# Optimization experiments

Measured on AMD Instinct MI355X. Metric: run time of the kernel, lower is better.

## Reference

```python
import jax, jax.numpy as jnp
import numpy as np

N_NODES = 100000
N_EDGES = 500000
H = 128

def _mlp(x, w1, b1, w2, b2):
    return jax.nn.relu(x @ w1 + b1) @ w2 + b2

def setup_inputs() -> dict:
    key = jax.random.key(0)
    ks = jax.random.split(key, 20)
    s = lambda fan_in: 1.0 / np.sqrt(fan_in)
    inp = {
        'x': jax.random.normal(ks[0], (N_NODES, H), jnp.float32),
        'edge_index': jax.random.randint(ks[1], (2, N_EDGES), 0, N_NODES, jnp.int64),
        'edge_attr': jax.random.normal(ks[2], (N_EDGES, H), jnp.float32),
        # edge_mlp: Linear(3h->h), ReLU, Linear(h->h); weights stored [in,out]
        'ew1': jax.random.uniform(ks[3], (3 * H, H), jnp.float32, -s(3 * H), s(3 * H)),
        'eb1': jnp.zeros((H,), jnp.float32),
        'ew2': jax.random.uniform(ks[4], (H, H), jnp.float32, -s(H), s(H)),
        'eb2': jnp.zeros((H,), jnp.float32),
        # node_mlp_phi: Linear(2h->h), ReLU, Linear(h->h)
        'pw1': jax.random.uniform(ks[5], (2 * H, H), jnp.float32, -s(2 * H), s(2 * H)),
        'pb1': jnp.zeros((H,), jnp.float32),
        'pw2': jax.random.uniform(ks[6], (H, H), jnp.float32, -s(H), s(H)),
        'pb2': jnp.zeros((H,), jnp.float32),
        # node_mlp_gamma: Linear(2h->h), ReLU, Linear(h->h)
        'gw1': jax.random.uniform(ks[7], (2 * H, H), jnp.float32, -s(2 * H), s(2 * H)),
        'gb1': jnp.zeros((H,), jnp.float32),
        'gw2': jax.random.uniform(ks[8], (H, H), jnp.float32, -s(H), s(H)),
        'gb2': jnp.zeros((H,), jnp.float32),
        # node_mlp_beta: Linear(h->h), ReLU, Linear(h->h)
        'bw1': jax.random.uniform(ks[9], (H, H), jnp.float32, -s(H), s(H)),
        'bb1': jnp.zeros((H,), jnp.float32),
        'bw2': jax.random.uniform(ks[10], (H, H), jnp.float32, -s(H), s(H)),
        'bb2': jnp.zeros((H,), jnp.float32),
    }
    return inp

def reference(x, edge_index, edge_attr, ew1, eb1, ew2, eb2, pw1, pb1, pw2, pb2,
              gw1, gb1, gw2, gb2, bw1, bb1, bw2, bb2):
    n = x.shape[0]
    row, col = edge_index[0], edge_index[1]
    x_row = x[row]            # [E, h]
    x_col = x[col]            # [E, h]
    edge_feat = jnp.concatenate([x_row, x_col, edge_attr], axis=1)  # [E, 3h]
    new_edge_attr = _mlp(edge_feat, ew1, eb1, ew2, eb2)             # [E, h]
    messages = _mlp(jnp.concatenate([x_col, new_edge_attr], axis=1), pw1, pb1, pw2, pb2)  # [E, h]
    # scatter_mean over row -> [N, h]
    sums = jax.ops.segment_sum(messages, row, num_segments=n)
    counts = jax.ops.segment_sum(jnp.ones((messages.shape[0],), messages.dtype), row, num_segments=n)
    agg = sums / jnp.maximum(counts, 1.0)[:, None]
    node_feat = jnp.concatenate([x, agg], axis=1)                   # [N, 2h]
    x_new = _mlp(node_feat, gw1, gb1, gw2, gb2)
    x_new = x_new + _mlp(x_new, bw1, bb1, bw2, bb2)
    return (x_new, new_edge_attr)
```

## Files before the change

### kernel.cpp

```cpp
#include <hip/hip_runtime.h>
#include <hip/hip_bf16.h>

typedef float f32x4 __attribute__((ext_vector_type(4)));
typedef short bf16x8 __attribute__((ext_vector_type(8)));
typedef unsigned short u16;
typedef unsigned short u16x4 __attribute__((ext_vector_type(4)));

#define HDIM 128
#define NNODES 100000
#define NEDGES 500000

#define WT_OFF   0
#define P1_OFF   393216
#define P2_OFF   (P1_OFF + 25600000)
#define Q_OFF    (P2_OFF + 25600000)
#define SUMS_OFF (Q_OFF + 25600000)
#define CNT_OFF  (SUMS_OFF + 51200000)

__device__ __forceinline__ u16 f2bf(float f) {
  unsigned int u = __builtin_bit_cast(unsigned int, f);
  u += 0x7fffu + ((u >> 16) & 1u);
  return (u16)(u >> 16);
}
__device__ __forceinline__ float bf2f(u16 h) {
  unsigned int u = ((unsigned int)h) << 16;
  return __builtin_bit_cast(float, u);
}

__device__ __forceinline__ u16* lds_at(u16* base, int row, int colBytes) {
  return (u16*)((char*)base + row * 256 + (colBytes ^ ((row & 7) << 4)));
}

__device__ __forceinline__ void stage_weight(const u16* __restrict__ wsrc, u16* wb, int tid) {
#pragma unroll
  for (int i = 0; i < 8; ++i) {
    int q = tid + 256 * i;
    int r = q >> 4, c = q & 15;
    uint4 v = *(const uint4*)(wsrc + r * 128 + c * 8);
    *(uint4*)lds_at(wb, r, c * 16) = v;
  }
}

__device__ __forceinline__ void wave_gemm(u16* aBuf, u16* wb, f32x4* acc, int lane, int wv) {
  const int arow = 16 * wv + (lane & 15);
  const int kg = (lane >> 4) * 16;
#pragma unroll
  for (int ks = 0; ks < 4; ++ks) {
    bf16x8 a = *(const bf16x8*)lds_at(aBuf, arow, ks * 64 + kg);
#pragma unroll
    for (int nt = 0; nt < 8; ++nt) {
      bf16x8 b = *(const bf16x8*)lds_at(wb, nt * 16 + (lane & 15), ks * 64 + kg);
      acc[nt] = __builtin_amdgcn_mfma_f32_16x16x32_bf16(a, b, acc[nt], 0, 0, 0);
    }
  }
}

__global__ __launch_bounds__(256) void k_prep(
    const float* __restrict__ ew1, const float* __restrict__ ew2,
    const float* __restrict__ pw1, const float* __restrict__ pw2,
    const float* __restrict__ gw1, const float* __restrict__ gw2,
    const float* __restrict__ bw1, const float* __restrict__ bw2,
    u16* __restrict__ WT) {
  int m = blockIdx.x;
  const float* src; int k0 = 0;
  switch (m) {
    case 0: src = ew1; k0 = 0;   break;
    case 1: src = ew1; k0 = 128; break;
    case 2: src = ew1; k0 = 256; break;
    case 3: src = ew2; break;
    case 4: src = pw1; break;
    case 5: src = pw1; k0 = 128; break;
    case 6: src = pw2; break;
    case 7: src = gw1; break;
    case 8: src = gw1; k0 = 128; break;
    case 9: src = gw2; break;
    case 10: src = bw1; break;
    default: src = bw2; break;
  }
  for (int i = 0; i < 64; ++i) {
    int idx = threadIdx.x + 256 * i;
    int n = idx & 127, k = idx >> 7;
    WT[m * 16384 + n * 128 + k] = f2bf(src[(k0 + k) * 128 + n]);
  }
}

__global__ __launch_bounds__(256) void k_node_pre(
    const float* __restrict__ x, const u16* __restrict__ WT,
    const float* __restrict__ eb1, const float* __restrict__ pb1,
    u16* __restrict__ P1, u16* __restrict__ P2, u16* __restrict__ Qm) {
  __shared__ u16 smem[32768];
  u16* wb = smem; u16* bufX = smem + 16384; u16* bufO = smem + 24576;
  const int tid = threadIdx.x, lane = tid & 63, wv = tid >> 6;
  const int nbase = blockIdx.x * 64 + 16 * wv;
#pragma unroll
  for (int i = 0; i < 8; ++i) {
    int q = lane + 64 * i; int r = q >> 5, c4 = q & 31; int n = nbase + r;
    float4 v = make_float4(0.f, 0.f, 0.f, 0.f);
    if (n < NNODES) v = *(const float4*)(x + (size_t)n * HDIM + c4 * 4);
    u16x4 h = { f2bf(v.x), f2bf(v.y), f2bf(v.z), f2bf(v.w) };
    *(u16x4*)lds_at(bufX, 16 * wv + r, c4 * 8) = h;
  }
#pragma unroll 1
  for (int job = 0; job < 3; ++job) {
    int m = (job == 0) ? 0 : (job == 1) ? 1 : 4;
    const float* bias = (job == 0) ? eb1 : (job == 1) ? nullptr : pb1;
    u16* out = (job == 0) ? P1 : (job == 1) ? P2 : Qm;
    __syncthreads();
    stage_weight(WT + m * 16384, wb, tid);
    __syncthreads();
    f32x4 acc[8] = {};
    wave_gemm(bufX, wb, acc, lane, wv);
#pragma unroll
    for (int nt = 0; nt < 8; ++nt) {
      int col = nt * 16 + (lane & 15);
      float bv = bias ? bias[col] : 0.0f;
#pragma unroll
      for (int j = 0; j < 4; ++j) {
        int r = 4 * (lane >> 4) + j;
        *lds_at(bufO, 16 * wv + r, col * 2) = f2bf(acc[nt][j] + bv);
      }
    }
#pragma unroll
    for (int i = 0; i < 4; ++i) {
      int q = lane + 64 * i; int r = q >> 4, c = q & 15; int n = nbase + r;
      if (n < NNODES)
        *(bf16x8*)(out + (size_t)n * HDIM + c * 8) =
            *(const bf16x8*)lds_at(bufO, 16 * wv + r, c * 16);
    }
  }
}

__global__ __launch_bounds__(256) void k_edge(
    const float* __restrict__ attr, const int* __restrict__ eidx,
    const u16* __restrict__ WT, const u16* __restrict__ P1,
    const u16* __restrict__ P2, const u16* __restrict__ Qm,
    const float* __restrict__ eb2, float* __restrict__ sums,
    float* __restrict__ counts, float* __restrict__ outNE) {
  __shared__ u16 smem[32768];
  u16* wb = smem; u16* bufA = smem + 16384; u16* bufH = smem + 24576;
  const int tid = threadIdx.x, lane = tid & 63, wv = tid >> 6;
  const int e0 = blockIdx.x * 64;
  const int ebase = e0 + 16 * wv;
  if (tid < 64 && e0 + tid < NEDGES) atomicAdd(&counts[eidx[e0 + tid]], 1.0f);
#pragma unroll
  for (int i = 0; i < 8; ++i) {
    int q = lane + 64 * i; int r = q >> 5, c4 = q & 31; int e = ebase + r;
    float4 v = make_float4(0.f, 0.f, 0.f, 0.f);
    if (e < NEDGES) v = *(const float4*)(attr + (size_t)e * HDIM + c4 * 4);
    u16x4 h = { f2bf(v.x), f2bf(v.y), f2bf(v.z), f2bf(v.w) };
    *(u16x4*)lds_at(bufA, 16 * wv + r, c4 * 8) = h;
  }
  stage_weight(WT + 2 * 16384, wb, tid);
  __syncthreads();
  f32x4 acc[8] = {};
  wave_gemm(bufA, wb, acc, lane, wv);
#pragma unroll
  for (int i = 0; i < 4; ++i) {
    int q = lane + 64 * i; int r = q >> 4, cc = (q & 15) * 8; int e = ebase + r;
    bf16x8 res = {};
    if (e < NEDGES) {
      int rid = eidx[e], cid = eidx[NEDGES + e];
      bf16x8 a = *(const bf16x8*)(P1 + (size_t)rid * HDIM + cc);
      bf16x8 b = *(const bf16x8*)(P2 + (size_t)cid * HDIM + cc);
#pragma unroll
      for (int k = 0; k < 8; ++k)
        res[k] = (short)f2bf(bf2f((u16)a[k]) + bf2f((u16)b[k]));
    }
    *(bf16x8*)lds_at(bufH, 16 * wv + r, cc * 2) = res;
  }
#pragma unroll
  for (int nt = 0; nt < 8; ++nt) {
#pragma unroll
    for (int j = 0; j < 4; ++j) {
      int r = 4 * (lane >> 4) + j; int cb = (nt * 16 + (lane & 15)) * 2;
      u16* p = lds_at(bufH, 16 * wv + r, cb);
      float v = acc[nt][j] + bf2f(*p);
      *p = f2bf(fmaxf(v, 0.0f));
    }
  }
  __syncthreads();
  stage_weight(WT + 3 * 16384, wb, tid);
  __syncthreads();
#pragma unroll
  for (int t = 0; t < 8; ++t) acc[t] = (f32x4){0.f, 0.f, 0.f, 0.f};
  wave_gemm(bufH, wb, acc, lane, wv);
#pragma unroll
  for (int nt = 0; nt < 8; ++nt) {
    int col = nt * 16 + (lane & 15);
    float bias = eb2[col];
#pragma unroll
    for (int j = 0; j < 4; ++j) {
      int r = 4 * (lane >> 4) + j; int e = ebase + r;
      float v = acc[nt][j] + bias;
      *lds_at(bufA, 16 * wv + r, col * 2) = f2bf(v);
      if (e < NEDGES) outNE[(size_t)e * HDIM + col] = v;
    }
  }
#pragma unroll
  for (int i = 0; i < 4; ++i) {
    int q = lane + 64 * i; int r = q >> 4, cc = (q & 15) * 8; int e = ebase + r;
    bf16x8 res = {};
    if (e < NEDGES) res = *(const bf16x8*)(Qm + (size_t)eidx[NEDGES + e] * HDIM + cc);
    *(bf16x8*)lds_at(bufH, 16 * wv + r, cc * 2) = res;
  }
  __syncthreads();
  stage_weight(WT + 5 * 16384, wb, tid);
  __syncthreads();
#pragma unroll
  for (int t = 0; t < 8; ++t) acc[t] = (f32x4){0.f, 0.f, 0.f, 0.f};
  wave_gemm(bufA, wb, acc, lane, wv);
  int rid4[4];
#pragma unroll
  for (int j = 0; j < 4; ++j) {
    int e = ebase + 4 * (lane >> 4) + j;
    rid4[j] = (e < NEDGES) ? eidx[e] : -1;
  }
#pragma unroll
  for (int nt = 0; nt < 8; ++nt) {
    int col = nt * 16 + (lane & 15);
#pragma unroll
    for (int j = 0; j < 4; ++j) {
      if (rid4[j] >= 0) {
        int r = 4 * (lane >> 4) + j;
        float v = acc[nt][j] + bf2f(*lds_at(bufH, 16 * wv + r, col * 2));
        v = fmaxf(v, 0.0f);
        atomicAdd(&sums[(size_t)rid4[j] * HDIM + col], v);
      }
    }
  }
}

__global__ __launch_bounds__(256) void k_node(
    const float* __restrict__ x, const u16* __restrict__ WT,
    const float* __restrict__ sums, const float* __restrict__ counts,
    const float* __restrict__ pb2, const float* __restrict__ gb1,
    const float* __restrict__ gb2, const float* __restrict__ bb1,
    const float* __restrict__ bb2, float* __restrict__ dout) {
  __shared__ u16 smem[32768];
  u16* wb = smem; u16* bufA = smem + 16384; u16* bufH = smem + 24576;
  const int tid = threadIdx.x, lane = tid & 63, wv = tid >> 6;
  const int nbase = blockIdx.x * 64 + 16 * wv;
#pragma unroll
  for (int i = 0; i < 8; ++i) {
    int q = lane + 64 * i; int r = q >> 5, c4 = q & 31; int n = nbase + r;
    float4 v = make_float4(0.f, 0.f, 0.f, 0.f);
    if (n < NNODES) v = *(const float4*)(sums + (size_t)n * HDIM + c4 * 4);
    u16x4 h = { f2bf(v.x), f2bf(v.y), f2bf(v.z), f2bf(v.w) };
    *(u16x4*)lds_at(bufA, 16 * wv + r, c4 * 8) = h;
  }
  stage_weight(WT + 6 * 16384, wb, tid);
  __syncthreads();
  f32x4 acc[8] = {};
  wave_gemm(bufA, wb, acc, lane, wv);
  float cv[4];
#pragma unroll
  for (int j = 0; j < 4; ++j) {
    int n = nbase + 4 * (lane >> 4) + j;
    cv[j] = (n < NNODES) ? counts[n] : 0.0f;
  }
#pragma unroll
  for (int nt = 0; nt < 8; ++nt) {
    int col = nt * 16 + (lane & 15);
    float bias = pb2[col];
#pragma unroll
    for (int j = 0; j < 4; ++j) {
      int r = 4 * (lane >> 4) + j;
      float v = (cv[j] >= 1.0f) ? (acc[nt][j] / cv[j] + bias) : 0.0f;
      *lds_at(bufH, 16 * wv + r, col * 2) = f2bf(v);
    }
  }
#pragma unroll
  for (int i = 0; i < 8; ++i) {
    int q = lane + 64 * i; int r = q >> 5, c4 = q & 31; int n = nbase + r;
    float4 v = make_float4(0.f, 0.f, 0.f, 0.f);
    if (n < NNODES) v = *(const float4*)(x + (size_t)n * HDIM + c4 * 4);
    u16x4 h = { f2bf(v.x), f2bf(v.y), f2bf(v.z), f2bf(v.w) };
    *(u16x4*)lds_at(bufA, 16 * wv + r, c4 * 8) = h;
  }
  __syncthreads();
  stage_weight(WT + 7 * 16384, wb, tid);
  __syncthreads();
  f32x4 acc2[8] = {};
  wave_gemm(bufA, wb, acc2, lane, wv);
  __syncthreads();
  stage_weight(WT + 8 * 16384, wb, tid);
  __syncthreads();
  wave_gemm(bufH, wb, acc2, lane, wv);
#pragma unroll
  for (int nt = 0; nt < 8; ++nt) {
    int col = nt * 16 + (lane & 15);
    float bias = gb1[col];
#pragma unroll
    for (int j = 0; j < 4; ++j) {
      int r = 4 * (lane >> 4) + j;
      *lds_at(bufH, 16 * wv + r, col * 2) = f2bf(fmaxf(acc2[nt][j] + bias, 0.0f));
    }
  }
  __syncthreads();
  stage_weight(WT + 9 * 16384, wb, tid);
  __syncthreads();
  f32x4 accX[8] = {};
  wave_gemm(bufH, wb, accX, lane, wv);
#pragma unroll
  for (int nt = 0; nt < 8; ++nt) {
    int col = nt * 16 + (lane & 15);
    float bias = gb2[col];
#pragma unroll
    for (int j = 0; j < 4; ++j) {
      int r = 4 * (lane >> 4) + j;
      accX[nt][j] += bias;
      *lds_at(bufA, 16 * wv + r, col * 2) = f2bf(accX[nt][j]);
    }
  }
  __syncthreads();
  stage_weight(WT + 10 * 16384, wb, tid);
  __syncthreads();
  f32x4 acc3[8] = {};
  wave_gemm(bufA, wb, acc3, lane, wv);
#pragma unroll
  for (int nt = 0; nt < 8; ++nt) {
    int col = nt * 16 + (lane & 15);
    float bias = bb1[col];
#pragma unroll
    for (int j = 0; j < 4; ++j) {
      int r = 4 * (lane >> 4) + j;
      *lds_at(bufH, 16 * wv + r, col * 2) = f2bf(fmaxf(acc3[nt][j] + bias, 0.0f));
    }
  }
  __syncthreads();
  stage_weight(WT + 11 * 16384, wb, tid);
  __syncthreads();
  f32x4 acc4[8] = {};
  wave_gemm(bufH, wb, acc4, lane, wv);
#pragma unroll
  for (int nt = 0; nt < 8; ++nt) {
    int col = nt * 16 + (lane & 15);
    float bias = bb2[col];
#pragma unroll
    for (int j = 0; j < 4; ++j) {
      int n = nbase + 4 * (lane >> 4) + j;
      if (n < NNODES) dout[(size_t)n * HDIM + col] = accX[nt][j] + acc4[nt][j] + bias;
    }
  }
}

extern "C" void kernel_launch(void* const* d_in, const int* in_sizes, int n_in,
                              void* d_out, int out_size, void* d_ws, size_t ws_size,
                              hipStream_t stream) {
  (void)in_sizes; (void)n_in; (void)out_size; (void)ws_size;
  const float* x   = (const float*)d_in[0];
  const int* eidx  = (const int*)d_in[1];
  const float* attr= (const float*)d_in[2];
  const float* ew1 = (const float*)d_in[3];
  const float* eb1 = (const float*)d_in[4];
  const float* ew2 = (const float*)d_in[5];
  const float* eb2 = (const float*)d_in[6];
  const float* pw1 = (const float*)d_in[7];
  const float* pb1 = (const float*)d_in[8];
  const float* pw2 = (const float*)d_in[9];
  const float* pb2 = (const float*)d_in[10];
  const float* gw1 = (const float*)d_in[11];
  const float* gb1 = (const float*)d_in[12];
  const float* gw2 = (const float*)d_in[13];
  const float* gb2 = (const float*)d_in[14];
  const float* bw1 = (const float*)d_in[15];
  const float* bb1 = (const float*)d_in[16];
  const float* bw2 = (const float*)d_in[17];
  const float* bb2 = (const float*)d_in[18];

  char* ws = (char*)d_ws;
  u16* WT   = (u16*)(ws + WT_OFF);
  u16* P1   = (u16*)(ws + P1_OFF);
  u16* P2   = (u16*)(ws + P2_OFF);
  u16* Qm   = (u16*)(ws + Q_OFF);
  float* sums   = (float*)(ws + SUMS_OFF);
  float* counts = (float*)(ws + CNT_OFF);
  float* xnew_out = (float*)d_out;
  float* ne_out   = (float*)d_out + (size_t)NNODES * HDIM;

  hipMemsetAsync(ws + SUMS_OFF, 0, 51200000 + 400000, stream);
  k_prep<<<12, 256, 0, stream>>>(ew1, ew2, pw1, pw2, gw1, gw2, bw1, bw2, WT);
  k_node_pre<<<1563, 256, 0, stream>>>(x, WT, eb1, pb1, P1, P2, Qm);
  k_edge<<<7813, 256, 0, stream>>>(attr, eidx, WT, P1, P2, Qm, eb2, sums, counts, ne_out);
  k_node<<<1563, 256, 0, stream>>>(x, WT, sums, counts, pb2, gb1, gb2, bb1, bb2, xnew_out);
}
```

Before: 1.066 ms.

## Read weights from global in MFMA loop, use packed fp16 atomics for sums

The GEMM helper now loads weight fragments straight from global memory (served by L1/L2) instead of staging each 128x128 weight into LDS. This removes the staging loops and many __syncthreads, and halves LDS use per block, which may allow more resident blocks. The scatter-sum accumulator becomes fp16 with global_atomic_pk_add_f16, halving atomic count and the memset size, at the cost of fp16 accumulation precision and range. The weight-prep kernel is also parallelized over 96 blocks with vectorized stores.

```diff
diff --git a/kernel.cpp b/kernel.cpp
--- a/kernel.cpp
+++ b/kernel.cpp
@@ -1,5 +1,6 @@
 #include <hip/hip_runtime.h>
 #include <hip/hip_bf16.h>
+#include <hip/hip_fp16.h>
 
 typedef float f32x4 __attribute__((ext_vector_type(4)));
 typedef short bf16x8 __attribute__((ext_vector_type(8)));
@@ -15,7 +16,7 @@
 #define P2_OFF   (P1_OFF + 25600000)
 #define Q_OFF    (P2_OFF + 25600000)
 #define SUMS_OFF (Q_OFF + 25600000)
-#define CNT_OFF  (SUMS_OFF + 51200000)
+#define CNT_OFF  (SUMS_OFF + 25600000)
 
 __device__ __forceinline__ u16 f2bf(float f) {
   unsigned int u = __builtin_bit_cast(unsigned int, f);
@@ -31,25 +32,20 @@
   return (u16*)((char*)base + row * 256 + (colBytes ^ ((row & 7) << 4)));
 }
 
-__device__ __forceinline__ void stage_weight(const u16* __restrict__ wsrc, u16* wb, int tid) {
-#pragma unroll
-  for (int i = 0; i < 8; ++i) {
-    int q = tid + 256 * i;
-    int r = q >> 4, c = q & 15;
-    uint4 v = *(const uint4*)(wsrc + r * 128 + c * 8);
-    *(uint4*)lds_at(wb, r, c * 16) = v;
-  }
-}
-
-__device__ __forceinline__ void wave_gemm(u16* aBuf, u16* wb, f32x4* acc, int lane, int wv) {
-  const int arow = 16 * wv + (lane & 15);
-  const int kg = (lane >> 4) * 16;
+__device__ __forceinline__ void atomic_pk_add_f16(__half* addr, unsigned int data) {
+  asm volatile("global_atomic_pk_add_f16 %0, %1, off" :: "v"(addr), "v"(data) : "memory");
+}
+
+__device__ __forceinline__ void wave_gemm_g(u16* aBuf, const u16* __restrict__ wt,
+                                            f32x4* acc, int lane, int wv) {
+  const int m = lane & 15, kq = lane >> 4;
+  const int arow = 16 * wv + m;
 #pragma unroll
   for (int ks = 0; ks < 4; ++ks) {
-    bf16x8 a = *(const bf16x8*)lds_at(aBuf, arow, ks * 64 + kg);
+    bf16x8 a = *(const bf16x8*)lds_at(aBuf, arow, ks * 64 + kq * 16);
 #pragma unroll
     for (int nt = 0; nt < 8; ++nt) {
-      bf16x8 b = *(const bf16x8*)lds_at(wb, nt * 16 + (lane & 15), ks * 64 + kg);
+      bf16x8 b = *(const bf16x8*)(wt + (size_t)(nt * 16 + m) * 128 + ks * 32 + kq * 8);
       acc[nt] = __builtin_amdgcn_mfma_f32_16x16x32_bf16(a, b, acc[nt], 0, 0, 0);
     }
   }
@@ -61,7 +57,7 @@
     const float* __restrict__ gw1, const float* __restrict__ gw2,
     const float* __restrict__ bw1, const float* __restrict__ bw2,
     u16* __restrict__ WT) {
-  int m = blockIdx.x;
+  int m = blockIdx.x >> 3;
   const float* src; int k0 = 0;
   switch (m) {
     case 0: src = ew1; k0 = 0;   break;
@@ -77,19 +73,21 @@
     case 10: src = bw1; break;
     default: src = bw2; break;
   }
-  for (int i = 0; i < 64; ++i) {
-    int idx = threadIdx.x + 256 * i;
-    int n = idx & 127, k = idx >> 7;
-    WT[m * 16384 + n * 128 + k] = f2bf(src[(k0 + k) * 128 + n]);
-  }
+  int c = (blockIdx.x & 7) * 256 + threadIdx.x;
+  int n = c >> 4, kc = c & 15;
+  u16 w8[8];
+#pragma unroll
+  for (int t = 0; t < 8; ++t)
+    w8[t] = f2bf(src[(size_t)(k0 + kc * 8 + t) * 128 + n]);
+  *(uint4*)(WT + m * 16384 + n * 128 + kc * 8) = *(const uint4*)w8;
 }
 
 __global__ __launch_bounds__(256) void k_node_pre(
     const float* __restrict__ x, const u16* __restrict__ WT,
     const float* __restrict__ eb1, const float* __restrict__ pb1,
     u16* __restrict__ P1, u16* __restrict__ P2, u16* __restrict__ Qm) {
-  __shared__ u16 smem[32768];
-  u16* wb = smem; u16* bufX = smem + 16384; u16* bufO = smem + 24576;
+  __shared__ u16 smem[16384];
+  u16* bufX = smem; u16* bufO = smem + 8192;
   const int tid = threadIdx.x, lane = tid & 63, wv = tid >> 6;
   const int nbase = blockIdx.x * 64 + 16 * wv;
 #pragma unroll
@@ -102,14 +100,11 @@
   }
 #pragma unroll 1
   for (int job = 0; job < 3; ++job) {
-    int m = (job == 0) ? 0 : (job == 1) ? 1 : 4;
+    int mw = (job == 0) ? 0 : (job == 1) ? 1 : 4;
     const float* bias = (job == 0) ? eb1 : (job == 1) ? nullptr : pb1;
     u16* out = (job == 0) ? P1 : (job == 1) ? P2 : Qm;
-    __syncthreads();
-    stage_weight(WT + m * 16384, wb, tid);
-    __syncthreads();
     f32x4 acc[8] = {};
-    wave_gemm(bufX, wb, acc, lane, wv);
+    wave_gemm_g(bufX, WT + mw * 16384, acc, lane, wv);
 #pragma unroll
     for (int nt = 0; nt < 8; ++nt) {
       int col = nt * 16 + (lane & 15);
@@ -134,10 +129,10 @@
     const float* __restrict__ attr, const int* __restrict__ eidx,
     const u16* __restrict__ WT, const u16* __restrict__ P1,
     const u16* __restrict__ P2, const u16* __restrict__ Qm,
-    const float* __restrict__ eb2, float* __restrict__ sums,
+    const float* __restrict__ eb2, __half* __restrict__ sums,
     float* __restrict__ counts, float* __restrict__ outNE) {
-  __shared__ u16 smem[32768];
-  u16* wb = smem; u16* bufA = smem + 16384; u16* bufH = smem + 24576;
+  __shared__ u16 smem[16384];
+  u16* bufA = smem; u16* bufH = smem + 8192;
   const int tid = threadIdx.x, lane = tid & 63, wv = tid >> 6;
   const int e0 = blockIdx.x * 64;
   const int ebase = e0 + 16 * wv;
@@ -150,10 +145,8 @@
     u16x4 h = { f2bf(v.x), f2bf(v.y), f2bf(v.z), f2bf(v.w) };
     *(u16x4*)lds_at(bufA, 16 * wv + r, c4 * 8) = h;
   }
-  stage_weight(WT + 2 * 16384, wb, tid);
-  __syncthreads();
   f32x4 acc[8] = {};
-  wave_gemm(bufA, wb, acc, lane, wv);
+  wave_gemm_g(bufA, WT + 2 * 16384, acc, lane, wv);
 #pragma unroll
   for (int i = 0; i < 4; ++i) {
     int q = lane + 64 * i; int r = q >> 4, cc = (q & 15) * 8; int e = ebase + r;
@@ -178,12 +171,9 @@
       *p = f2bf(fmaxf(v, 0.0f));
     }
   }
-  __syncthreads();
-  stage_weight(WT + 3 * 16384, wb, tid);
-  __syncthreads();
 #pragma unroll
   for (int t = 0; t < 8; ++t) acc[t] = (f32x4){0.f, 0.f, 0.f, 0.f};
-  wave_gemm(bufH, wb, acc, lane, wv);
+  wave_gemm_g(bufH, WT + 3 * 16384, acc, lane, wv);
 #pragma unroll
   for (int nt = 0; nt < 8; ++nt) {
     int col = nt * 16 + (lane & 15);
@@ -203,12 +193,9 @@
     if (e < NEDGES) res = *(const bf16x8*)(Qm + (size_t)eidx[NEDGES + e] * HDIM + cc);
     *(bf16x8*)lds_at(bufH, 16 * wv + r, cc * 2) = res;
   }
-  __syncthreads();
-  stage_weight(WT + 5 * 16384, wb, tid);
-  __syncthreads();
 #pragma unroll
   for (int t = 0; t < 8; ++t) acc[t] = (f32x4){0.f, 0.f, 0.f, 0.f};
-  wave_gemm(bufA, wb, acc, lane, wv);
+  wave_gemm_g(bufA, WT + 5 * 16384, acc, lane, wv);
   int rid4[4];
 #pragma unroll
   for (int j = 0; j < 4; ++j) {
@@ -220,11 +207,16 @@
     int col = nt * 16 + (lane & 15);
 #pragma unroll
     for (int j = 0; j < 4; ++j) {
-      if (rid4[j] >= 0) {
-        int r = 4 * (lane >> 4) + j;
-        float v = acc[nt][j] + bf2f(*lds_at(bufH, 16 * wv + r, col * 2));
-        v = fmaxf(v, 0.0f);
-        atomicAdd(&sums[(size_t)rid4[j] * HDIM + col], v);
+      int r = 4 * (lane >> 4) + j;
+      float v = acc[nt][j] + bf2f(*lds_at(bufH, 16 * wv + r, col * 2));
+      v = fmaxf(v, 0.0f);
+      float other = __shfl_xor(v, 1);
+      if (((lane & 1) == (j & 1)) && rid4[j] >= 0) {
+        float lo = ((lane & 1) == 0) ? v : other;
+        float hi = ((lane & 1) == 0) ? other : v;
+        __half2 h2 = __floats2half2_rn(lo, hi);
+        atomic_pk_add_f16(sums + (size_t)rid4[j] * HDIM + (col & ~1),
+                          __builtin_bit_cast(unsigned int, h2));
       }
     }
   }
@@ -232,26 +224,31 @@
 
 __global__ __launch_bounds__(256) void k_node(
     const float* __restrict__ x, const u16* __restrict__ WT,
-    const float* __restrict__ sums, const float* __restrict__ counts,
+    const __half* __restrict__ sums, const float* __restrict__ counts,
     const float* __restrict__ pb2, const float* __restrict__ gb1,
     const float* __restrict__ gb2, const float* __restrict__ bb1,
     const float* __restrict__ bb2, float* __restrict__ dout) {
-  __shared__ u16 smem[32768];
-  u16* wb = smem; u16* bufA = smem + 16384; u16* bufH = smem + 24576;
+  __shared__ u16 smem[16384];
+  u16* bufA = smem; u16* bufH = smem + 8192;
   const int tid = threadIdx.x, lane = tid & 63, wv = tid >> 6;
   const int nbase = blockIdx.x * 64 + 16 * wv;
 #pragma unroll
-  for (int i = 0; i < 8; ++i) {
-    int q = lane + 64 * i; int r = q >> 5, c4 = q & 31; int n = nbase + r;
-    float4 v = make_float4(0.f, 0.f, 0.f, 0.f);
-    if (n < NNODES) v = *(const float4*)(sums + (size_t)n * HDIM + c4 * 4);
-    u16x4 h = { f2bf(v.x), f2bf(v.y), f2bf(v.z), f2bf(v.w) };
-    *(u16x4*)lds_at(bufA, 16 * wv + r, c4 * 8) = h;
-  }
-  stage_weight(WT + 6 * 16384, wb, tid);
-  __syncthreads();
+  for (int i = 0; i < 4; ++i) {
+    int q = lane + 64 * i; int r = q >> 4, c8 = q & 15; int n = nbase + r;
+    bf16x8 h = {};
+    if (n < NNODES) {
+      const __half2* sp = (const __half2*)(sums + (size_t)n * HDIM + c8 * 8);
+#pragma unroll
+      for (int t = 0; t < 4; ++t) {
+        float2 f = __half22float2(sp[t]);
+        h[2 * t]     = (short)f2bf(f.x);
+        h[2 * t + 1] = (short)f2bf(f.y);
+      }
+    }
+    *(bf16x8*)lds_at(bufA, 16 * wv + r, c8 * 16) = h;
+  }
   f32x4 acc[8] = {};
-  wave_gemm(bufA, wb, acc, lane, wv);
+  wave_gemm_g(bufA, WT + 6 * 16384, acc, lane, wv);
   float cv[4];
 #pragma unroll
   for (int j = 0; j < 4; ++j) {
@@ -277,15 +274,9 @@
     u16x4 h = { f2bf(v.x), f2bf(v.y), f2bf(v.z), f2bf(v.w) };
     *(u16x4*)lds_at(bufA, 16 * wv + r, c4 * 8) = h;
   }
-  __syncthreads();
-  stage_weight(WT + 7 * 16384, wb, tid);
-  __syncthreads();
   f32x4 acc2[8] = {};
-  wave_gemm(bufA, wb, acc2, lane, wv);
-  __syncthreads();
-  stage_weight(WT + 8 * 16384, wb, tid);
-  __syncthreads();
-  wave_gemm(bufH, wb, acc2, lane, wv);
+  wave_gemm_g(bufA, WT + 7 * 16384, acc2, lane, wv);
+  wave_gemm_g(bufH, WT + 8 * 16384, acc2, lane, wv);
 #pragma unroll
   for (int nt = 0; nt < 8; ++nt) {
     int col = nt * 16 + (lane & 15);
@@ -296,11 +287,8 @@
       *lds_at(bufH, 16 * wv + r, col * 2) = f2bf(fmaxf(acc2[nt][j] + bias, 0.0f));
     }
   }
-  __syncthreads();
-  stage_weight(WT + 9 * 16384, wb, tid);
-  __syncthreads();
   f32x4 accX[8] = {};
-  wave_gemm(bufH, wb, accX, lane, wv);
+  wave_gemm_g(bufH, WT + 9 * 16384, accX, lane, wv);
 #pragma unroll
   for (int nt = 0; nt < 8; ++nt) {
     int col = nt * 16 + (lane & 15);
@@ -312,11 +300,8 @@
       *lds_at(bufA, 16 * wv + r, col * 2) = f2bf(accX[nt][j]);
     }
   }
-  __syncthreads();
-  stage_weight(WT + 10 * 16384, wb, tid);
-  __syncthreads();
   f32x4 acc3[8] = {};
-  wave_gemm(bufA, wb, acc3, lane, wv);
+  wave_gemm_g(bufA, WT + 10 * 16384, acc3, lane, wv);
 #pragma unroll
   for (int nt = 0; nt < 8; ++nt) {
     int col = nt * 16 + (lane & 15);
@@ -327,11 +312,8 @@
       *lds_at(bufH, 16 * wv + r, col * 2) = f2bf(fmaxf(acc3[nt][j] + bias, 0.0f));
     }
   }
-  __syncthreads();
-  stage_weight(WT + 11 * 16384, wb, tid);
-  __syncthreads();
   f32x4 acc4[8] = {};
-  wave_gemm(bufH, wb, acc4, lane, wv);
+  wave_gemm_g(bufH, WT + 11 * 16384, acc4, lane, wv);
 #pragma unroll
   for (int nt = 0; nt < 8; ++nt) {
     int col = nt * 16 + (lane & 15);
@@ -373,13 +355,13 @@
   u16* P1   = (u16*)(ws + P1_OFF);
   u16* P2   = (u16*)(ws + P2_OFF);
   u16* Qm   = (u16*)(ws + Q_OFF);
-  float* sums   = (float*)(ws + SUMS_OFF);
+  __half* sums  = (__half*)(ws + SUMS_OFF);
   float* counts = (float*)(ws + CNT_OFF);
   float* xnew_out = (float*)d_out;
   float* ne_out   = (float*)d_out + (size_t)NNODES * HDIM;
 
-  hipMemsetAsync(ws + SUMS_OFF, 0, 51200000 + 400000, stream);
-  k_prep<<<12, 256, 0, stream>>>(ew1, ew2, pw1, pw2, gw1, gw2, bw1, bw2, WT);
+  hipMemsetAsync(ws + SUMS_OFF, 0, 25600000 + 400000, stream);
+  k_prep<<<96, 256, 0, stream>>>(ew1, ew2, pw1, pw2, gw1, gw2, bw1, bw2, WT);
   k_node_pre<<<1563, 256, 0, stream>>>(x, WT, eb1, pb1, P1, P2, Qm);
   k_edge<<<7813, 256, 0, stream>>>(attr, eidx, WT, P1, P2, Qm, eb2, sums, counts, ne_out);
   k_node<<<1563, 256, 0, stream>>>(x, WT, sums, counts, pb2, gb1, gb2, bb1, bb2, xnew_out);
```

Result: slower. 1.363 ms (+27.9%).
